# Kernel tuning notes

Measured on AMD Instinct MI355X. Metric: run time of the kernel, lower is better.

## Reference

```python
import jax, jax.numpy as jnp
import numpy as np

B, N, D, H, DM = 4, 1024, 1024, 16, 4096
DH = D // H
SCALE = DH ** -0.5
EPS = 1e-5


def layer_norm(x, g, b):
    mu = jnp.mean(x, axis=-1, keepdims=True)
    var = jnp.mean((x - mu) ** 2, axis=-1, keepdims=True)
    return (x - mu) * jax.lax.rsqrt(var + EPS) * g + b


def mha(q_in, k_in, v_in, Wq, bq, Wk, bk, Wv, bv, Wp, bp):
    # weights stored (in, out); torch Linear equivalent y = x @ W + b
    q = (q_in @ Wq + bq).reshape(B, -1, H, DH).transpose(0, 2, 1, 3)  # (B,H,Nq,DH)
    k = (k_in @ Wk + bk).reshape(B, -1, H, DH).transpose(0, 2, 1, 3)
    v = (v_in @ Wv + bv).reshape(B, -1, H, DH).transpose(0, 2, 1, 3)
    attn = jax.nn.softmax(jnp.einsum('bhqd,bhkd->bhqk', q, k) * SCALE, axis=-1)
    x = jnp.einsum('bhqk,bhkd->bhqd', attn, v).transpose(0, 2, 1, 3).reshape(B, -1, D)
    return x @ Wp + bp


def setup_inputs() -> dict:
    key = jax.random.key(0)
    ks = jax.random.split(key, 32)
    s = 0.02
    inp = {
        'tokens_enc': jax.random.normal(ks[0], (B, N, D), jnp.float32),
        'tokens_dec': jax.random.normal(ks[1], (B, N, D), jnp.float32),
        'PE_enc': jax.random.normal(ks[2], (B, N, D), jnp.float32),
        'PE_dec': jax.random.normal(ks[3], (B, N, D), jnp.float32),
    }
    names = ['sa_Wq', 'sa_Wk', 'sa_Wv', 'sa_Wp', 'ca_Wq', 'ca_Wk', 'ca_Wv', 'ca_Wp']
    for i, n in enumerate(names):
        inp[n] = jax.random.normal(ks[4 + i], (D, D), jnp.float32) * s
        inp[n.replace('W', 'b')] = jnp.zeros((D,), jnp.float32)
    inp['mlp_W1'] = jax.random.normal(ks[12], (D, DM), jnp.float32) * s
    inp['mlp_b1'] = jnp.zeros((DM,), jnp.float32)
    inp['mlp_W2'] = jax.random.normal(ks[13], (DM, D), jnp.float32) * s
    inp['mlp_b2'] = jnp.zeros((D,), jnp.float32)
    for i in (1, 2, 3):
        inp[f'ln{i}_g'] = jnp.ones((D,), jnp.float32)
        inp[f'ln{i}_b'] = jnp.zeros((D,), jnp.float32)
    return inp


def reference(tokens_enc, tokens_dec, PE_enc, PE_dec,
              sa_Wq, sa_bq, sa_Wk, sa_bk, sa_Wv, sa_bv, sa_Wp, sa_bp,
              ca_Wq, ca_bq, ca_Wk, ca_bk, ca_Wv, ca_bv, ca_Wp, ca_bp,
              mlp_W1, mlp_b1, mlp_W2, mlp_b2,
              ln1_g, ln1_b, ln2_g, ln2_b, ln3_g, ln3_b):
    # SA (pre-norm): q=k=ln(x)+PE_dec, v=ln(x)
    x2 = layer_norm(tokens_dec, ln1_g, ln1_b)
    qk = x2 + PE_dec
    tokens_dec = tokens_dec + mha(qk, qk, x2, sa_Wq, sa_bq, sa_Wk, sa_bk, sa_Wv, sa_bv, sa_Wp, sa_bp)
    # CA: q=ln(x)+PE_dec, k=enc+PE_enc, v=enc
    x2 = layer_norm(tokens_dec, ln2_g, ln2_b)
    tokens_dec = tokens_dec + mha(x2 + PE_dec, tokens_enc + PE_enc, tokens_enc,
                                  ca_Wq, ca_bq, ca_Wk, ca_bk, ca_Wv, ca_bv, ca_Wp, ca_bp)
    # FFD
    x2 = layer_norm(tokens_dec, ln3_g, ln3_b)
    h = jax.nn.gelu(x2 @ mlp_W1 + mlp_b1, approximate=False)
    return tokens_dec + (h @ mlp_W2 + mlp_b2)
```

## Files before the change

kernel.cpp:

```cpp
#include <hip/hip_runtime.h>
#include <hip/hip_bf16.h>
#include <math.h>

#define B_ 4
#define N_ 1024
#define D_ 1024
#define H_ 16
#define DH_ 64
#define DM_ 4096
#define NT_ (B_*N_)
#define EPS_ 1e-5f
#define SCALE_ 0.125f
#define CEXP_ 0.1803368801111244f

typedef unsigned short u16;
typedef short s16x8 __attribute__((ext_vector_type(8)));
typedef __bf16 y16x8 __attribute__((ext_vector_type(8)));
typedef float f32x4 __attribute__((ext_vector_type(4)));
typedef float f32x16 __attribute__((ext_vector_type(16)));

#define ZERO16 (f32x16){0.f,0.f,0.f,0.f,0.f,0.f,0.f,0.f,0.f,0.f,0.f,0.f,0.f,0.f,0.f,0.f}

__device__ __forceinline__ u16 f2bs(float f) {
  unsigned int u = __builtin_bit_cast(unsigned int, f);
  u += 0x7fffu + ((u >> 16) & 1u);
  return (u16)(u >> 16);
}

static __device__ __forceinline__ f32x4 MFMA(y16x8 a, y16x8 b, f32x4 c) {
  return __builtin_amdgcn_mfma_f32_16x16x32_bf16(a, b, c, 0, 0, 0);
}
static __device__ __forceinline__ f32x16 MFMA32(y16x8 a, y16x8 b, f32x16 c) {
  return __builtin_amdgcn_mfma_f32_32x32x16_bf16(a, b, c, 0, 0, 0);
}

static __device__ __forceinline__ unsigned cvtpk(float a, float b) {
  unsigned r;
  asm("v_cvt_pk_bf16_f32 %0, %1, %2" : "=v"(r) : "v"(a), "v"(b));
  return r;
}

static __device__ __forceinline__ void async16(void* lds, const void* g) {
  __builtin_amdgcn_global_load_lds(
      (const __attribute__((address_space(1))) unsigned int*)g,
      (__attribute__((address_space(3))) unsigned int*)lds, 16, 0, 0);
}

__global__ __launch_bounds__(256) void k_wtrans8(
    const float* __restrict__ s0, const float* __restrict__ s1,
    const float* __restrict__ s2, const float* __restrict__ s3,
    const float* __restrict__ s4, const float* __restrict__ s5,
    const float* __restrict__ s6, const float* __restrict__ s7,
    u16* __restrict__ dst) {
  const float* srcs[8] = {s0, s1, s2, s3, s4, s5, s6, s7};
  const float* W = srcs[blockIdx.z];
  u16* Wt = dst + (size_t)blockIdx.z * D_ * D_;
  __shared__ u16 tile[32][33];
  int n0 = blockIdx.x * 32, k0 = blockIdx.y * 32;
  int tx = threadIdx.x & 31, ty = threadIdx.x >> 5;
#pragma unroll
  for (int i = 0; i < 4; ++i) {
    int k = k0 + ty + i * 8;
    tile[ty + i * 8][tx] = f2bs(W[(size_t)k * D_ + n0 + tx]);
  }
  __syncthreads();
#pragma unroll
  for (int i = 0; i < 4; ++i) {
    int n = n0 + ty + i * 8;
    Wt[(size_t)n * D_ + k0 + tx] = tile[tx][ty + i * 8];
  }
}

__global__ __launch_bounds__(256) void k_wtrans(const float* __restrict__ W,
                                                u16* __restrict__ Wt,
                                                int K, int Ncols) {
  __shared__ u16 tile[32][33];
  int n0 = blockIdx.x * 32, k0 = blockIdx.y * 32;
  int tx = threadIdx.x & 31, ty = threadIdx.x >> 5;
#pragma unroll
  for (int i = 0; i < 4; ++i) {
    int k = k0 + ty + i * 8;
    tile[ty + i * 8][tx] = f2bs(W[(size_t)k * Ncols + n0 + tx]);
  }
  __syncthreads();
#pragma unroll
  for (int i = 0; i < 4; ++i) {
    int n = n0 + ty + i * 8;
    Wt[(size_t)n * K + k0 + tx] = tile[tx][ty + i * 8];
  }
}

__global__ __launch_bounds__(256) void k_encprep(const float* __restrict__ enc,
                                                 const float* __restrict__ pe,
                                                 u16* __restrict__ encpe,
                                                 u16* __restrict__ encv) {
  int i = blockIdx.x * 256 + threadIdx.x;
  float4 e = ((const float4*)enc)[i];
  float4 p = ((const float4*)pe)[i];
  union { u16 u[4]; uint2 v; } a, b;
  a.u[0] = f2bs(e.x + p.x); a.u[1] = f2bs(e.y + p.y);
  a.u[2] = f2bs(e.z + p.z); a.u[3] = f2bs(e.w + p.w);
  b.u[0] = f2bs(e.x); b.u[1] = f2bs(e.y); b.u[2] = f2bs(e.z); b.u[3] = f2bs(e.w);
  ((uint2*)encpe)[i] = a.v;
  ((uint2*)encv)[i] = b.v;
}

__global__ __launch_bounds__(256) void k_ln(const float* __restrict__ x,
                                            const float* __restrict__ g,
                                            const float* __restrict__ bta,
                                            const float* __restrict__ pe,
                                            u16* __restrict__ x2o,
                                            u16* __restrict__ qko) {
  int row = blockIdx.x;
  int t = threadIdx.x;
  float4 v = ((const float4*)(x + (size_t)row * D_))[t];
  float s = v.x + v.y + v.z + v.w;
#pragma unroll
  for (int o = 1; o < 64; o <<= 1) s += __shfl_xor(s, o, 64);
  __shared__ float red[8];
  if ((t & 63) == 0) red[t >> 6] = s;
  __syncthreads();
  float mean = (red[0] + red[1] + red[2] + red[3]) * (1.0f / D_);
  float dx = v.x - mean, dy = v.y - mean, dz = v.z - mean, dw = v.w - mean;
  float s2 = dx * dx + dy * dy + dz * dz + dw * dw;
#pragma unroll
  for (int o = 1; o < 64; o <<= 1) s2 += __shfl_xor(s2, o, 64);
  if ((t & 63) == 0) red[4 + (t >> 6)] = s2;
  __syncthreads();
  float var = (red[4] + red[5] + red[6] + red[7]) * (1.0f / D_);
  float rstd = rsqrtf(var + EPS_);
  float4 gv = ((const float4*)g)[t];
  float4 bv = ((const float4*)bta)[t];
  float y0 = dx * rstd * gv.x + bv.x;
  float y1 = dy * rstd * gv.y + bv.y;
  float y2 = dz * rstd * gv.z + bv.z;
  float y3 = dw * rstd * gv.w + bv.w;
  union { u16 u[4]; uint2 v2; } o1;
  o1.u[0] = f2bs(y0); o1.u[1] = f2bs(y1); o1.u[2] = f2bs(y2); o1.u[3] = f2bs(y3);
  ((uint2*)(x2o + (size_t)row * D_))[t] = o1.v2;
  if (pe) {
    float4 pv = ((const float4*)(pe + (size_t)row * D_))[t];
    union { u16 u[4]; uint2 v2; } o2;
    o2.u[0] = f2bs(y0 + pv.x); o2.u[1] = f2bs(y1 + pv.y);
    o2.u[2] = f2bs(y2 + pv.z); o2.u[3] = f2bs(y3 + pv.w);
    ((uint2*)(qko + (size_t)row * D_))[t] = o2.v2;
  }
}

template <int EPI>
__global__ __launch_bounds__(512) void k_gemm(const u16* __restrict__ A,
                                              const u16* __restrict__ Bt,
                                              const float* __restrict__ bias,
                                              const float* __restrict__ res,
                                              float* __restrict__ outf,
                                              u16* __restrict__ outb,
                                              int M, int Nn, int K, int ldo) {
  constexpr int BM = 128, BN = 128, BK = 64;
  __shared__ __align__(128) char smem[2][(BM + BN) * BK * 2];
  const int t = threadIdx.x;
  const int wave = t >> 6, lane = t & 63, lg = lane >> 4, lc = lane & 15;
  const int nwg = gridDim.x * gridDim.y;
  const int bid = blockIdx.y * gridDim.x + blockIdx.x;
  const int lb = (bid & 7) * (nwg >> 3) + (bid >> 3);
  const int bx = lb % gridDim.x, by = lb / gridDim.x;
  const int m0 = by * BM, n0 = bx * BN;
  const int wm = (wave >> 2) * 64, wn = (wave & 3) * 32;
  f32x4 acc[4][2];
#pragma unroll
  for (int i = 0; i < 4; ++i)
#pragma unroll
    for (int j = 0; j < 2; ++j) acc[i][j] = (f32x4){0.f, 0.f, 0.f, 0.f};
  const char* Ag = (const char*)(A + (size_t)m0 * K);
  const char* Bg = (const char*)(Bt + (size_t)n0 * K);
  const int sr = t >> 3, sp = t & 7;

  auto stage = [&](int bufi, int kt) {
    char* sA = smem[bufi];
    char* sB = smem[bufi] + BM * BK * 2;
#pragma unroll
    for (int rr = 0; rr < 2; ++rr) {
      int row = rr * 64 + sr;
      int c = sp ^ (row & 7);
      async16(sA + (size_t)row * 128 + sp * 16,
              Ag + ((size_t)row * K + kt + c * 8) * 2);
      async16(sB + (size_t)row * 128 + sp * 16,
              Bg + ((size_t)row * K + kt + c * 8) * 2);
    }
  };
  auto compute = [&](int bufi) {
    const char* sA = smem[bufi];
    const char* sB = smem[bufi] + BM * BK * 2;
#pragma unroll
    for (int ks = 0; ks < 2; ++ks) {
      y16x8 af[4], bfr[2];
#pragma unroll
      for (int fm = 0; fm < 4; ++fm) {
        int R = wm + fm * 16 + lc;
        int pc = (ks * 4 + lg) ^ (R & 7);
        af[fm] = *(const y16x8*)(sA + (size_t)R * 128 + pc * 16);
      }
#pragma unroll
      for (int fn = 0; fn < 2; ++fn) {
        int R = wn + fn * 16 + lc;
        int pc = (ks * 4 + lg) ^ (R & 7);
        bfr[fn] = *(const y16x8*)(sB + (size_t)R * 128 + pc * 16);
      }
#pragma unroll
      for (int fm = 0; fm < 4; ++fm)
#pragma unroll
        for (int fn = 0; fn < 2; ++fn)
          acc[fm][fn] = MFMA(af[fm], bfr[fn], acc[fm][fn]);
    }
  };

  stage(0, 0);
  __syncthreads();
  int cur = 0;
  for (int kt = BK; kt < K; kt += BK) {
    stage(cur ^ 1, kt);
    compute(cur);
    __syncthreads();
    cur ^= 1;
  }
  compute(cur);

#pragma unroll
  for (int fm = 0; fm < 4; ++fm)
#pragma unroll
    for (int fn = 0; fn < 2; ++fn)
#pragma unroll
      for (int j = 0; j < 4; ++j) {
        int row = m0 + wm + fm * 16 + lg * 4 + j;
        int col = n0 + wn + fn * 16 + lc;
        float vv = acc[fm][fn][j] + bias[col];
        size_t idx = (size_t)row * ldo + col;
        if constexpr (EPI == 0) {
          outb[idx] = f2bs(vv);
        } else if constexpr (EPI == 1) {
          outf[idx] = vv + res[idx];
        } else {
          float gx = 0.5f * vv * (1.0f + erff(vv * 0.70710678118f));
          outb[idx] = f2bs(gx);
        }
      }
}

__global__ __launch_bounds__(512) void k_gemmG(
    const u16* __restrict__ A0, const u16* __restrict__ A1,
    const u16* __restrict__ A2, const u16* __restrict__ W0,
    const u16* __restrict__ W1, const u16* __restrict__ W2,
    const float* __restrict__ b0, const float* __restrict__ b1,
    const float* __restrict__ b2, u16* __restrict__ outqk,
    u16* __restrict__ outvt) {
  constexpr int BM = 128, BN = 128, BK = 64, K = D_;
  __shared__ __align__(128) char smem[2][(BM + BN) * BK * 2];
  const int z = blockIdx.z;
  const u16* A = z == 0 ? A0 : (z == 1 ? A1 : A2);
  const u16* Bt = z == 0 ? W0 : (z == 1 ? W1 : W2);
  const float* bias = z == 0 ? b0 : (z == 1 ? b1 : b2);
  const int t = threadIdx.x;
  const int wave = t >> 6, lane = t & 63, lg = lane >> 4, lc = lane & 15;
  const int nwg = gridDim.x * gridDim.y;
  const int bid = blockIdx.y * gridDim.x + blockIdx.x;
  const int lb = (bid & 7) * (nwg >> 3) + (bid >> 3);
  const int bx = lb % gridDim.x, by = lb / gridDim.x;
  const int m0 = by * BM, n0 = bx * BN;
  const int wm = (wave >> 2) * 64, wn = (wave & 3) * 32;
  f32x4 acc[4][2];
#pragma unroll
  for (int i = 0; i < 4; ++i)
#pragma unroll
    for (int j = 0; j < 2; ++j) acc[i][j] = (f32x4){0.f, 0.f, 0.f, 0.f};
  const char* Ag = (const char*)(A + (size_t)m0 * K);
  const char* Bg = (const char*)(Bt + (size_t)n0 * K);
  const int sr = t >> 3, sp = t & 7;

  auto stage = [&](int bufi, int kt) {
    char* sA = smem[bufi];
    char* sB = smem[bufi] + BM * BK * 2;
#pragma unroll
    for (int rr = 0; rr < 2; ++rr) {
      int row = rr * 64 + sr;
      int c = sp ^ (row & 7);
      async16(sA + (size_t)row * 128 + sp * 16,
              Ag + ((size_t)row * K + kt + c * 8) * 2);
      async16(sB + (size_t)row * 128 + sp * 16,
              Bg + ((size_t)row * K + kt + c * 8) * 2);
    }
  };
  auto compute = [&](int bufi) {
    const char* sA = smem[bufi];
    const char* sB = smem[bufi] + BM * BK * 2;
#pragma unroll
    for (int ks = 0; ks < 2; ++ks) {
      y16x8 af[4], bfr[2];
#pragma unroll
      for (int fm = 0; fm < 4; ++fm) {
        int R = wm + fm * 16 + lc;
        int pc = (ks * 4 + lg) ^ (R & 7);
        af[fm] = *(const y16x8*)(sA + (size_t)R * 128 + pc * 16);
      }
#pragma unroll
      for (int fn = 0; fn < 2; ++fn) {
        int R = wn + fn * 16 + lc;
        int pc = (ks * 4 + lg) ^ (R & 7);
        bfr[fn] = *(const y16x8*)(sB + (size_t)R * 128 + pc * 16);
      }
#pragma unroll
      for (int fm = 0; fm < 4; ++fm)
#pragma unroll
        for (int fn = 0; fn < 2; ++fn)
          acc[fm][fn] = MFMA(af[fm], bfr[fn], acc[fm][fn]);
    }
  };

  stage(0, 0);
  __syncthreads();
  int cur = 0;
  for (int kt = BK; kt < K; kt += BK) {
    stage(cur ^ 1, kt);
    compute(cur);
    __syncthreads();
    cur ^= 1;
  }
  compute(cur);

  if (z < 2) {
#pragma unroll
    for (int fm = 0; fm < 4; ++fm)
#pragma unroll
      for (int fn = 0; fn < 2; ++fn)
#pragma unroll
        for (int j = 0; j < 4; ++j) {
          int row = m0 + wm + fm * 16 + lg * 4 + j;
          int col = n0 + wn + fn * 16 + lc;
          outqk[(size_t)row * (2 * D_) + z * D_ + col] =
              f2bs(acc[fm][fn][j] + bias[col]);
        }
  } else {
#pragma unroll
    for (int fm = 0; fm < 4; ++fm)
#pragma unroll
      for (int fn = 0; fn < 2; ++fn) {
        int row0 = m0 + wm + fm * 16 + lg * 4;
        int col = n0 + wn + fn * 16 + lc;
        int bb = row0 >> 10, nn = row0 & (N_ - 1);
        int h = col >> 6, dh = col & 63;
        float bcol = bias[col];
        union { u16 u[4]; uint2 v; } pk;
#pragma unroll
        for (int j = 0; j < 4; ++j) pk.u[j] = f2bs(acc[fm][fn][j] + bcol);
        *(uint2*)&outvt[(((size_t)bb * H_ + h) * DH_ + dh) * N_ + nn] = pk.v;
      }
  }
}

__global__ __launch_bounds__(256) void k_attn(const u16* __restrict__ q, int qs,
                                              const u16* __restrict__ k, int ks2,
                                              const u16* __restrict__ vt,
                                              u16* __restrict__ out) {
  __shared__ __align__(16) u16 Kl[64][64];
  __shared__ __align__(16) u16 Vl[64][64];
  __shared__ __align__(16) u16 Ol[4][32][72];
  const int lb = blockIdx.x;
  const int bh = (lb & 7) | ((lb >> 6) << 3);
  const int qb = (lb >> 3) & 7;
  const int b = bh >> 4, h = bh & 15;
  const int t = threadIdx.x, wave = t >> 6, lane = t & 63;
  const int ql = lane & 31, hi = lane >> 5;
  const int q0 = qb * 128 + wave * 32;
  const u16* qp = q + ((size_t)b * N_ + q0) * qs + h * DH_;
  const u16* kp = k + (size_t)b * N_ * ks2 + h * DH_;
  const u16* vp = vt + ((size_t)bh * DH_) * N_;

  y16x8 aq[4];
#pragma unroll
  for (int s = 0; s < 4; ++s)
    aq[s] = *(const y16x8*)(qp + (size_t)ql * qs + s * 16 + hi * 8);

  f32x16 o0 = ZERO16, o1 = ZERO16;
  float m_r = -1e30f, l_r = 0.f;

  for (int kt = 0; kt < N_; kt += 64) {
    __syncthreads();
#pragma unroll
    for (int rr = 0; rr < 2; ++rr) {
      int id = rr * 256 + t;
      int row = id >> 3, c = id & 7;
      int pc2 = c ^ (row & 7);
      *(s16x8*)&Kl[row][pc2 * 8] =
          *(const s16x8*)(kp + (size_t)(kt + row) * ks2 + c * 8);
      *(s16x8*)&Vl[row][pc2 * 8] =
          *(const s16x8*)(vp + (size_t)row * N_ + kt + c * 8);
    }
    __syncthreads();

    f32x16 st0 = ZERO16, st1 = ZERO16;
#pragma unroll
    for (int s = 0; s < 4; ++s) {
      int pc0 = ((s * 2 + hi) ^ (ql & 7)) * 8;
      y16x8 ak0 = *(const y16x8*)&Kl[ql][pc0];
      y16x8 ak1 = *(const y16x8*)&Kl[32 + ql][pc0];
      st0 = MFMA32(ak0, aq[s], st0);
      st1 = MFMA32(ak1, aq[s], st1);
    }

    float mx = st0[0];
#pragma unroll
    for (int r = 1; r < 16; ++r) mx = fmaxf(mx, st0[r]);
#pragma unroll
    for (int r = 0; r < 16; ++r) mx = fmaxf(mx, st1[r]);
    mx = fmaxf(mx, __shfl_xor(mx, 32, 64));
    float mn = fmaxf(m_r, mx);
    float corr = exp2f((m_r - mn) * CEXP_);
    float ps = 0.f;
#pragma unroll
    for (int r = 0; r < 16; ++r) {
      float e = exp2f((st0[r] - mn) * CEXP_); st0[r] = e; ps += e;
    }
#pragma unroll
    for (int r = 0; r < 16; ++r) {
      float e = exp2f((st1[r] - mn) * CEXP_); st1[r] = e; ps += e;
    }
    ps += __shfl_xor(ps, 32, 64);
    l_r = l_r * corr + ps;
    m_r = mn;
    o0 = o0 * corr;
    o1 = o1 * corr;

#pragma unroll
    for (int ks = 0; ks < 4; ++ks) {
      unsigned A0, A1, B0, B1;
      if (ks < 2) {
        const int il = ks * 8;
        A0 = cvtpk(st0[il + 0], st0[il + 1]);
        A1 = cvtpk(st0[il + 2], st0[il + 3]);
        B0 = cvtpk(st0[il + 4], st0[il + 5]);
        B1 = cvtpk(st0[il + 6], st0[il + 7]);
      } else {
        const int il = (ks - 2) * 8;
        A0 = cvtpk(st1[il + 0], st1[il + 1]);
        A1 = cvtpk(st1[il + 2], st1[il + 3]);
        B0 = cvtpk(st1[il + 4], st1[il + 5]);
        B1 = cvtpk(st1[il + 6], st1[il + 7]);
      }
      asm("v_permlane32_swap_b32 %0, %1" : "+v"(A0), "+v"(B0));
      asm("v_permlane32_swap_b32 %0, %1" : "+v"(A1), "+v"(B1));
      union { unsigned w[4]; y16x8 v; } fr;
      fr.w[0] = A0; fr.w[1] = A1; fr.w[2] = B0; fr.w[3] = B1;
      int pc = ((ks * 2 + hi) ^ (ql & 7)) * 8;
      y16x8 bv0 = *(const y16x8*)&Vl[ql][pc];
      y16x8 bv1 = *(const y16x8*)&Vl[32 + ql][pc];
      o0 = MFMA32(bv0, fr.v, o0);
      o1 = MFMA32(bv1, fr.v, o1);
    }
  }

  float rl = 1.f / l_r;
#pragma unroll
  for (int rq = 0; rq < 4; ++rq)
#pragma unroll
    for (int e = 0; e < 4; e += 2) {
      *(unsigned*)&Ol[wave][ql][8 * rq + 4 * hi + e] =
          cvtpk(o0[rq * 4 + e] * rl, o0[rq * 4 + e + 1] * rl);
      *(unsigned*)&Ol[wave][ql][32 + 8 * rq + 4 * hi + e] =
          cvtpk(o1[rq * 4 + e] * rl, o1[rq * 4 + e + 1] * rl);
    }
#pragma unroll
  for (int pp = 0; pp < 4; ++pp) {
    int row = pp * 8 + (lane >> 3);
    s16x8 vv = *(const s16x8*)&Ol[wave][row][(lane & 7) * 8];
    *(s16x8*)(out + ((size_t)b * N_ + q0 + row) * D_ + h * DH_ + (lane & 7) * 8) = vv;
  }
}

extern "C" void kernel_launch(void* const* d_in, const int* in_sizes, int n_in,
                              void* d_out, int out_size, void* d_ws, size_t ws_size,
                              hipStream_t stream) {
  const float* tokens_enc = (const float*)d_in[0];
  const float* tokens_dec = (const float*)d_in[1];
  const float* PE_enc = (const float*)d_in[2];
  const float* PE_dec = (const float*)d_in[3];
  const float* sa_Wq = (const float*)d_in[4];  const float* sa_bq = (const float*)d_in[5];
  const float* sa_Wk = (const float*)d_in[6];  const float* sa_bk = (const float*)d_in[7];
  const float* sa_Wv = (const float*)d_in[8];  const float* sa_bv = (const float*)d_in[9];
  const float* sa_Wp = (const float*)d_in[10]; const float* sa_bp = (const float*)d_in[11];
  const float* ca_Wq = (const float*)d_in[12]; const float* ca_bq = (const float*)d_in[13];
  const float* ca_Wk = (const float*)d_in[14]; const float* ca_bk = (const float*)d_in[15];
  const float* ca_Wv = (const float*)d_in[16]; const float* ca_bv = (const float*)d_in[17];
  const float* ca_Wp = (const float*)d_in[18]; const float* ca_bp = (const float*)d_in[19];
  const float* mlp_W1 = (const float*)d_in[20]; const float* mlp_b1 = (const float*)d_in[21];
  const float* mlp_W2 = (const float*)d_in[22]; const float* mlp_b2 = (const float*)d_in[23];
  const float* ln1_g = (const float*)d_in[24]; const float* ln1_b = (const float*)d_in[25];
  const float* ln2_g = (const float*)d_in[26]; const float* ln2_b = (const float*)d_in[27];
  const float* ln3_g = (const float*)d_in[28]; const float* ln3_b = (const float*)d_in[29];

  char* wsp = (char*)d_ws;
  size_t off = 0;
  auto alloc = [&](size_t bytes) -> char* {
    char* p = wsp + off;
    off += (bytes + 255) & ~(size_t)255;
    return p;
  };
  u16* w8   = (u16*)alloc((size_t)8 * D_ * D_ * 2);
  u16* w1T  = (u16*)alloc((size_t)DM_ * D_ * 2);
  u16* w2T  = (u16*)alloc((size_t)D_ * DM_ * 2);
  u16* encpe = (u16*)alloc((size_t)NT_ * D_ * 2);
  u16* encv  = (u16*)alloc((size_t)NT_ * D_ * 2);
  u16* x2b = (u16*)alloc((size_t)NT_ * D_ * 2);
  u16* qkb = (u16*)alloc((size_t)NT_ * D_ * 2);
  u16* qkm = (u16*)alloc((size_t)NT_ * 2 * D_ * 2);
  u16* vtb = (u16*)alloc((size_t)NT_ * D_ * 2);
  u16* attb = (u16*)alloc((size_t)NT_ * D_ * 2);
  float* dec1 = (float*)alloc((size_t)NT_ * D_ * 4);
  float* dec2 = (float*)alloc((size_t)NT_ * D_ * 4);
  u16* hb = (u16*)alloc((size_t)NT_ * DM_ * 2);

  const size_t DD = (size_t)D_ * D_;
  u16* wqT  = w8;
  u16* wkT  = w8 + 1 * DD;
  u16* wvT  = w8 + 2 * DD;
  u16* wpT  = w8 + 3 * DD;
  u16* cwqT = w8 + 4 * DD;
  u16* cwkT = w8 + 5 * DD;
  u16* cwvT = w8 + 6 * DD;
  u16* cwpT = w8 + 7 * DD;

  k_wtrans8<<<dim3(32, 32, 8), 256, 0, stream>>>(sa_Wq, sa_Wk, sa_Wv, sa_Wp,
                                                 ca_Wq, ca_Wk, ca_Wv, ca_Wp, w8);
  k_wtrans<<<dim3(128, 32), 256, 0, stream>>>(mlp_W1, w1T, D_, DM_);
  k_wtrans<<<dim3(32, 128), 256, 0, stream>>>(mlp_W2, w2T, DM_, D_);
  k_encprep<<<dim3(NT_ * D_ / 1024), 256, 0, stream>>>(tokens_enc, PE_enc, encpe, encv);

  k_ln<<<dim3(NT_), 256, 0, stream>>>(tokens_dec, ln1_g, ln1_b, PE_dec, x2b, qkb);
  k_gemmG<<<dim3(8, 32, 3), 512, 0, stream>>>(qkb, qkb, x2b, wqT, wkT, wvT,
                                              sa_bq, sa_bk, sa_bv, qkm, vtb);
  k_attn<<<dim3(512), 256, 0, stream>>>(qkm, 2 * D_, qkm + D_, 2 * D_, vtb, attb);
  k_gemm<1><<<dim3(8, 32), 512, 0, stream>>>(attb, wpT, sa_bp, tokens_dec, dec1, nullptr, NT_, D_, D_, D_);

  k_ln<<<dim3(NT_), 256, 0, stream>>>(dec1, ln2_g, ln2_b, PE_dec, x2b, qkb);
  k_gemmG<<<dim3(8, 32, 3), 512, 0, stream>>>(qkb, encpe, encv, cwqT, cwkT, cwvT,
                                              ca_bq, ca_bk, ca_bv, qkm, vtb);
  k_attn<<<dim3(512), 256, 0, stream>>>(qkm, 2 * D_, qkm + D_, 2 * D_, vtb, attb);
  k_gemm<1><<<dim3(8, 32), 512, 0, stream>>>(attb, cwpT, ca_bp, dec1, dec2, nullptr, NT_, D_, D_, D_);

  k_ln<<<dim3(NT_), 256, 0, stream>>>(dec2, ln3_g, ln3_b, nullptr, x2b, nullptr);
  k_gemm<2><<<dim3(32, 32), 512, 0, stream>>>(x2b, w1T, mlp_b1, nullptr, nullptr, hb, NT_, DM_, D_, DM_);
  k_gemm<1><<<dim3(8, 32), 512, 0, stream>>>(hb, w2T, mlp_b2, dec2, (float*)d_out, nullptr, NT_, D_, DM_, D_);
}
```

Baseline: 355.3 us.

## Hoist cross-attention K/V projections into self-attention QKV launch; retile GEMMs

The cross-attention K and V projections depend only on encoder inputs, so they now run in the same batched launch as the self-attention Q/K/V projections (grid z=5), writing to separate buffers. The cross-attention Q projection runs as its own GEMM writing into the second buffer. The generic GEMM is replaced by a 256-thread, single-LDS-buffer variant with BN templated (64 for N=1024 outputs to double the block count, 128 for the MLP up-projection). This gives more parallelism for the narrow-output GEMMs and merges independent work into one launch. In exchange it drops the double-buffered global-to-LDS prefetch and adds an extra sync per K step.

```diff
diff --git a/kernel.cpp b/kernel.cpp
--- a/kernel.cpp
+++ b/kernel.cpp
@@ -52,8 +52,9 @@
     const float* __restrict__ s4, const float* __restrict__ s5,
     const float* __restrict__ s6, const float* __restrict__ s7,
     u16* __restrict__ dst) {
-  const float* srcs[8] = {s0, s1, s2, s3, s4, s5, s6, s7};
-  const float* W = srcs[blockIdx.z];
+  const float* W = blockIdx.z == 0 ? s0 : blockIdx.z == 1 ? s1 : blockIdx.z == 2 ? s2
+                 : blockIdx.z == 3 ? s3 : blockIdx.z == 4 ? s4 : blockIdx.z == 5 ? s5
+                 : blockIdx.z == 6 ? s6 : s7;
   u16* Wt = dst + (size_t)blockIdx.z * D_ * D_;
   __shared__ u16 tile[32][33];
   int n0 = blockIdx.x * 32, k0 = blockIdx.y * 32;
@@ -147,16 +148,17 @@
   }
 }
 
-template <int EPI>
-__global__ __launch_bounds__(512) void k_gemm(const u16* __restrict__ A,
-                                              const u16* __restrict__ Bt,
-                                              const float* __restrict__ bias,
-                                              const float* __restrict__ res,
-                                              float* __restrict__ outf,
-                                              u16* __restrict__ outb,
-                                              int M, int Nn, int K, int ldo) {
-  constexpr int BM = 128, BN = 128, BK = 64;
-  __shared__ __align__(128) char smem[2][(BM + BN) * BK * 2];
+template <int EPI, int BN>
+__global__ __launch_bounds__(256) void k_gemm2(const u16* __restrict__ A,
+                                               const u16* __restrict__ Bt,
+                                               const float* __restrict__ bias,
+                                               const float* __restrict__ res,
+                                               float* __restrict__ outf,
+                                               u16* __restrict__ outb,
+                                               int M, int Nn, int K, int ldo) {
+  constexpr int BM = 128, BK = 64;
+  constexpr int FN = BN / 32;
+  __shared__ __align__(128) char smem[(BM + BN) * BK * 2];
   const int t = threadIdx.x;
   const int wave = t >> 6, lane = t & 63, lg = lane >> 4, lc = lane & 15;
   const int nwg = gridDim.x * gridDim.y;
@@ -164,35 +166,38 @@
   const int lb = (bid & 7) * (nwg >> 3) + (bid >> 3);
   const int bx = lb % gridDim.x, by = lb / gridDim.x;
   const int m0 = by * BM, n0 = bx * BN;
-  const int wm = (wave >> 2) * 64, wn = (wave & 3) * 32;
-  f32x4 acc[4][2];
+  const int wm = (wave >> 1) * 64, wn = (wave & 1) * (BN / 2);
+  f32x4 acc[4][FN];
 #pragma unroll
   for (int i = 0; i < 4; ++i)
 #pragma unroll
-    for (int j = 0; j < 2; ++j) acc[i][j] = (f32x4){0.f, 0.f, 0.f, 0.f};
+    for (int j = 0; j < FN; ++j) acc[i][j] = (f32x4){0.f, 0.f, 0.f, 0.f};
   const char* Ag = (const char*)(A + (size_t)m0 * K);
   const char* Bg = (const char*)(Bt + (size_t)n0 * K);
+  char* sA = smem;
+  char* sB = smem + BM * BK * 2;
   const int sr = t >> 3, sp = t & 7;
 
-  auto stage = [&](int bufi, int kt) {
-    char* sA = smem[bufi];
-    char* sB = smem[bufi] + BM * BK * 2;
-#pragma unroll
-    for (int rr = 0; rr < 2; ++rr) {
-      int row = rr * 64 + sr;
+  for (int kt = 0; kt < K; kt += BK) {
+    __syncthreads();
+#pragma unroll
+    for (int rr = 0; rr < 4; ++rr) {
+      int row = rr * 32 + sr;
       int c = sp ^ (row & 7);
       async16(sA + (size_t)row * 128 + sp * 16,
               Ag + ((size_t)row * K + kt + c * 8) * 2);
+    }
+#pragma unroll
+    for (int rr = 0; rr < BN / 32; ++rr) {
+      int row = rr * 32 + sr;
+      int c = sp ^ (row & 7);
       async16(sB + (size_t)row * 128 + sp * 16,
               Bg + ((size_t)row * K + kt + c * 8) * 2);
     }
-  };
-  auto compute = [&](int bufi) {
-    const char* sA = smem[bufi];
-    const char* sB = smem[bufi] + BM * BK * 2;
+    __syncthreads();
 #pragma unroll
     for (int ks = 0; ks < 2; ++ks) {
-      y16x8 af[4], bfr[2];
+      y16x8 af[4], bfr[FN];
 #pragma unroll
       for (int fm = 0; fm < 4; ++fm) {
         int R = wm + fm * 16 + lc;
@@ -200,7 +205,7 @@
         af[fm] = *(const y16x8*)(sA + (size_t)R * 128 + pc * 16);
       }
 #pragma unroll
-      for (int fn = 0; fn < 2; ++fn) {
+      for (int fn = 0; fn < FN; ++fn) {
         int R = wn + fn * 16 + lc;
         int pc = (ks * 4 + lg) ^ (R & 7);
         bfr[fn] = *(const y16x8*)(sB + (size_t)R * 128 + pc * 16);
@@ -208,26 +213,15 @@
 #pragma unroll
       for (int fm = 0; fm < 4; ++fm)
 #pragma unroll
-        for (int fn = 0; fn < 2; ++fn)
+        for (int fn = 0; fn < FN; ++fn)
           acc[fm][fn] = MFMA(af[fm], bfr[fn], acc[fm][fn]);
     }
-  };
-
-  stage(0, 0);
-  __syncthreads();
-  int cur = 0;
-  for (int kt = BK; kt < K; kt += BK) {
-    stage(cur ^ 1, kt);
-    compute(cur);
-    __syncthreads();
-    cur ^= 1;
-  }
-  compute(cur);
+  }
 
 #pragma unroll
   for (int fm = 0; fm < 4; ++fm)
 #pragma unroll
-    for (int fn = 0; fn < 2; ++fn)
+    for (int fn = 0; fn < FN; ++fn)
 #pragma unroll
       for (int j = 0; j < 4; ++j) {
         int row = m0 + wm + fm * 16 + lg * 4 + j;
@@ -247,17 +241,20 @@
 
 __global__ __launch_bounds__(512) void k_gemmG(
     const u16* __restrict__ A0, const u16* __restrict__ A1,
-    const u16* __restrict__ A2, const u16* __restrict__ W0,
+    const u16* __restrict__ A2, const u16* __restrict__ A3,
+    const u16* __restrict__ A4, const u16* __restrict__ W0,
     const u16* __restrict__ W1, const u16* __restrict__ W2,
+    const u16* __restrict__ W3, const u16* __restrict__ W4,
     const float* __restrict__ b0, const float* __restrict__ b1,
-    const float* __restrict__ b2, u16* __restrict__ outqk,
-    u16* __restrict__ outvt) {
+    const float* __restrict__ b2, const float* __restrict__ b3,
+    const float* __restrict__ b4, u16* __restrict__ qk1,
+    u16* __restrict__ vt1, u16* __restrict__ qk2, u16* __restrict__ vt2) {
   constexpr int BM = 128, BN = 128, BK = 64, K = D_;
   __shared__ __align__(128) char smem[2][(BM + BN) * BK * 2];
   const int z = blockIdx.z;
-  const u16* A = z == 0 ? A0 : (z == 1 ? A1 : A2);
-  const u16* Bt = z == 0 ? W0 : (z == 1 ? W1 : W2);
-  const float* bias = z == 0 ? b0 : (z == 1 ? b1 : b2);
+  const u16* A = z == 0 ? A0 : z == 1 ? A1 : z == 2 ? A2 : z == 3 ? A3 : A4;
+  const u16* Bt = z == 0 ? W0 : z == 1 ? W1 : z == 2 ? W2 : z == 3 ? W3 : W4;
+  const float* bias = z == 0 ? b0 : z == 1 ? b1 : z == 2 ? b2 : z == 3 ? b3 : b4;
   const int t = threadIdx.x;
   const int wave = t >> 6, lane = t & 63, lg = lane >> 4, lc = lane & 15;
   const int nwg = gridDim.x * gridDim.y;
@@ -325,7 +322,10 @@
   }
   compute(cur);
 
-  if (z < 2) {
+  const bool isV = (z == 2) || (z == 4);
+  if (!isV) {
+    u16* outqk = (z == 3) ? qk2 : qk1;
+    const int coff = (z == 1 || z == 3) ? D_ : 0;
 #pragma unroll
     for (int fm = 0; fm < 4; ++fm)
 #pragma unroll
@@ -334,10 +334,11 @@
         for (int j = 0; j < 4; ++j) {
           int row = m0 + wm + fm * 16 + lg * 4 + j;
           int col = n0 + wn + fn * 16 + lc;
-          outqk[(size_t)row * (2 * D_) + z * D_ + col] =
+          outqk[(size_t)row * (2 * D_) + coff + col] =
               f2bs(acc[fm][fn][j] + bias[col]);
         }
   } else {
+    u16* outvt = (z == 2) ? vt1 : vt2;
 #pragma unroll
     for (int fm = 0; fm < 4; ++fm)
 #pragma unroll
@@ -510,7 +511,9 @@
   u16* x2b = (u16*)alloc((size_t)NT_ * D_ * 2);
   u16* qkb = (u16*)alloc((size_t)NT_ * D_ * 2);
   u16* qkm = (u16*)alloc((size_t)NT_ * 2 * D_ * 2);
+  u16* qkm2 = (u16*)alloc((size_t)NT_ * 2 * D_ * 2);
   u16* vtb = (u16*)alloc((size_t)NT_ * D_ * 2);
+  u16* vtb2 = (u16*)alloc((size_t)NT_ * D_ * 2);
   u16* attb = (u16*)alloc((size_t)NT_ * D_ * 2);
   float* dec1 = (float*)alloc((size_t)NT_ * D_ * 4);
   float* dec2 = (float*)alloc((size_t)NT_ * D_ * 4);
@@ -533,18 +536,23 @@
   k_encprep<<<dim3(NT_ * D_ / 1024), 256, 0, stream>>>(tokens_enc, PE_enc, encpe, encv);
 
   k_ln<<<dim3(NT_), 256, 0, stream>>>(tokens_dec, ln1_g, ln1_b, PE_dec, x2b, qkb);
-  k_gemmG<<<dim3(8, 32, 3), 512, 0, stream>>>(qkb, qkb, x2b, wqT, wkT, wvT,
-                                              sa_bq, sa_bk, sa_bv, qkm, vtb);
+  k_gemmG<<<dim3(8, 32, 5), 512, 0, stream>>>(
+      qkb, qkb, x2b, encpe, encv, wqT, wkT, wvT, cwkT, cwvT,
+      sa_bq, sa_bk, sa_bv, ca_bk, ca_bv, qkm, vtb, qkm2, vtb2);
   k_attn<<<dim3(512), 256, 0, stream>>>(qkm, 2 * D_, qkm + D_, 2 * D_, vtb, attb);
-  k_gemm<1><<<dim3(8, 32), 512, 0, stream>>>(attb, wpT, sa_bp, tokens_dec, dec1, nullptr, NT_, D_, D_, D_);
+  k_gemm2<1, 64><<<dim3(16, 32), 256, 0, stream>>>(attb, wpT, sa_bp, tokens_dec,
+                                                   dec1, nullptr, NT_, D_, D_, D_);
 
   k_ln<<<dim3(NT_), 256, 0, stream>>>(dec1, ln2_g, ln2_b, PE_dec, x2b, qkb);
-  k_gemmG<<<dim3(8, 32, 3), 512, 0, stream>>>(qkb, encpe, encv, cwqT, cwkT, cwvT,
-                                              ca_bq, ca_bk, ca_bv, qkm, vtb);
-  k_attn<<<dim3(512), 256, 0, stream>>>(qkm, 2 * D_, qkm + D_, 2 * D_, vtb, attb);
-  k_gemm<1><<<dim3(8, 32), 512, 0, stream>>>(attb, cwpT, ca_bp, dec1, dec2, nullptr, NT_, D_, D_, D_);
+  k_gemm2<0, 64><<<dim3(16, 32), 256, 0, stream>>>(qkb, cwqT, ca_bq, nullptr,
+                                                   nullptr, qkm2, NT_, D_, D_, 2 * D_);
+  k_attn<<<dim3(512), 256, 0, stream>>>(qkm2, 2 * D_, qkm2 + D_, 2 * D_, vtb2, attb);
+  k_gemm2<1, 64><<<dim3(16, 32), 256, 0, stream>>>(attb, cwpT, ca_bp, dec1,
+                                                   dec2, nullptr, NT_, D_, D_, D_);
 
   k_ln<<<dim3(NT_), 256, 0, stream>>>(dec2, ln3_g, ln3_b, nullptr, x2b, nullptr);
-  k_gemm<2><<<dim3(32, 32), 512, 0, stream>>>(x2b, w1T, mlp_b1, nullptr, nullptr, hb, NT_, DM_, D_, DM_);
-  k_gemm<1><<<dim3(8, 32), 512, 0, stream>>>(hb, w2T, mlp_b2, dec2, (float*)d_out, nullptr, NT_, D_, DM_, D_);
-}
+  k_gemm2<2, 128><<<dim3(32, 32), 256, 0, stream>>>(x2b, w1T, mlp_b1, nullptr,
+                                                    nullptr, hb, NT_, DM_, D_, DM_);
+  k_gemm2<1, 64><<<dim3(16, 32), 256, 0, stream>>>(hb, w2T, mlp_b2, dec2,
+                                                   (float*)d_out, nullptr, NT_, D_, DM_, D_);
+}
```

Measured after the change: 386.5 us. +8.8%, slower.
